# Optimization experiments

Measured on AMD Instinct MI355X. Metric: run time of the kernel, lower is better.

## Reference

```python
import jax, jax.numpy as jnp
import numpy as np

EPS = 1e-6

def setup_inputs() -> dict:
    key = jax.random.key(0)
    ks = jax.random.split(key, 12)
    B, C, H, W = 2, 192, 192, 192
    f = lambda k, s, sc=1.0: jax.random.normal(k, s, dtype=jnp.float32) * sc
    d = {}
    d["x_l"] = f(ks[0], (B, C, H, W))
    d["x_r"] = f(ks[1], (B, C, H, W))
    d["ln_l_w"] = jnp.ones((C,), jnp.float32)
    d["ln_l_b"] = jnp.zeros((C,), jnp.float32)
    d["ln_r_w"] = jnp.ones((C,), jnp.float32)
    d["ln_r_b"] = jnp.zeros((C,), jnp.float32)
    s = C ** -0.5
    d["wq_l"] = f(ks[2], (C, C), s)   # 1x1 conv weights as [out,in]
    d["wq_r"] = f(ks[3], (C, C), s)
    d["wv_l"] = f(ks[4], (C, C), s)
    d["wv_r"] = f(ks[5], (C, C), s)
    d["mlp_w1"] = f(ks[6], (C // 24, C // 3), (C // 3) ** -0.5)
    d["mlp_w2"] = f(ks[7], (C * 2 // 3, C // 24), (C // 24) ** -0.5)
    d["scale_h"] = jnp.ones((1,), jnp.float32)
    d["scale_w"] = jnp.ones((1,), jnp.float32)
    # layer scales are zero-init in the module; use small random so output is nontrivial
    d["ls1"] = f(ks[8], (1, C, 1, 1), 0.1)
    d["ls2"] = f(ks[9], (1, C, 1, 1), 0.1)
    return d

def _ln2d(x, w, b):
    # LayerNorm over channel dim of NCHW
    mu = x.mean(1, keepdims=True)
    var = ((x - mu) ** 2).mean(1, keepdims=True)
    return (x - mu) * jax.lax.rsqrt(var + EPS) * w[None, :, None, None] + b[None, :, None, None]

def _pw(x, w):
    # 1x1 conv, no bias
    return jnp.einsum('bchw,oc->bohw', x, w)

def reference(x_l, x_r, ln_l_w, ln_l_b, ln_r_w, ln_r_b, wq_l, wq_r, wv_l, wv_r,
              mlp_w1, mlp_w2, scale_h, scale_w, ls1, ls2):
    q_l_h, q_l_w, q_l_c = jnp.split(_pw(_ln2d(x_l, ln_l_w, ln_l_b), wq_l), 3, axis=1)
    q_r_h, q_r_w, q_r_c = jnp.split(_pw(_ln2d(x_r, ln_r_w, ln_r_b), wq_r), 3, axis=1)
    v_l_h, v_l_w, v_l_c = jnp.split(_pw(x_l, wv_l), 3, axis=1)
    v_r_h, v_r_w, v_r_c = jnp.split(_pw(x_r, wv_r), 3, axis=1)

    # height axial attention: scores [b, w, h, h']
    attn_h = jnp.einsum('bchw,bcgw->bwhg', q_l_h, q_r_h) * scale_h[0]
    attn_h = jax.nn.softmax(attn_h, axis=-1)
    x_r2l_h = jnp.einsum('bwhg,bcgw->bchw', attn_h, v_r_h)           # [b,c,h,w]
    x_l2r_h = jnp.einsum('bwhg,bchw->bcgw', attn_h, v_l_h)           # attn^T @ v_l

    # width axial attention: scores [b, h, w, w'] (softmax applied separately per direction)
    attn_w = jnp.einsum('bchw,bchv->bhwv', q_l_w, q_r_w) * scale_w[0]
    a1 = jax.nn.softmax(attn_w, axis=-1)
    x_r2l_w = jnp.einsum('bhwv,bchv->bchw', a1, v_r_w)
    a2 = jax.nn.softmax(jnp.swapaxes(attn_w, -1, -2), axis=-1)       # [b,h,v,w]
    x_l2r_w = jnp.einsum('bhvw,bchw->bchv', a2, v_l_w)

    # channel SE branch: sum of the two channel queries, GAP, bottleneck MLP
    p = (q_l_c + q_r_c).mean(axis=(2, 3))                            # [b, c]
    h1 = jax.nn.relu(p @ mlp_w1.T)                                   # [b, c//8]
    a = jax.nn.softmax(h1 @ mlp_w2.T, axis=1)                        # softmax over 2c channels jointly
    attn_l_c, attn_r_c = jnp.split(a, 2, axis=1)
    x_r2l_c = attn_l_c[:, :, None, None] * v_l_c
    x_l2r_c = attn_r_c[:, :, None, None] * v_r_c

    x_r2l = jnp.concatenate([x_r2l_h, x_r2l_w, x_r2l_c], axis=1)
    x_l2r = jnp.concatenate([x_l2r_h, x_l2r_w, x_l2r_c], axis=1)
    out_l = x_r2l * ls1 + x_l
    out_r = x_l2r * ls2 + x_r
    return (out_l, out_r)
```

## Files before the change

### kernel.cpp

```cpp
#include <hip/hip_runtime.h>
#include <stdint.h>

#define NN 36864
#define PL 7077888
#define PL64 2359296
#define TOT 14155776

typedef unsigned short ushort_t;
typedef __attribute__((ext_vector_type(8))) __bf16 bf16x8;
typedef __attribute__((ext_vector_type(4))) float f32x4;
typedef __attribute__((ext_vector_type(4))) unsigned int u32x4;

__device__ __forceinline__ ushort_t f2bf(float f) {
  unsigned int u = __builtin_bit_cast(unsigned int, f);
  u = (u + 0x7FFFu + ((u >> 16) & 1u)) >> 16;
  return (ushort_t)u;
}
__device__ __forceinline__ float bf2f(ushort_t h) {
  unsigned int u = ((unsigned int)h) << 16;
  return __builtin_bit_cast(float, u);
}
__device__ __forceinline__ bf16x8 lds8(const ushort_t* p) {
  return __builtin_bit_cast(bf16x8, *(const u32x4*)p);
}
__device__ __forceinline__ f32x4 mfma16(bf16x8 a, bf16x8 b, f32x4 c) {
  return __builtin_amdgcn_mfma_f32_16x16x32_bf16(a, b, c, 0, 0, 0);
}
__device__ __forceinline__ unsigned cvtpk(float lo, float hi) {
  unsigned r;
  asm("v_cvt_pk_bf16_f32 %0, %1, %2" : "=v"(r) : "v"(lo), "v"(hi));
  return r;
}

__global__ void k_prep(const float* __restrict__ wq, const float* __restrict__ wv,
                       const float* __restrict__ lnw, const float* __restrict__ lnb,
                       ushort_t* __restrict__ W, float* __restrict__ ab) {
  __shared__ float sa[3], sb[3];
  int r = blockIdx.x, t = threadIdx.x;
  if (r < 192) {
    float w  = wq[r*192 + t];
    float lw = lnw[t], lb = lnb[t];
    W[r*192 + t] = f2bf(w * lw);
    float av = w * lb, bv = -w * lw;
    #pragma unroll
    for (int off = 1; off < 64; off <<= 1) {
      av += __shfl_xor(av, off);
      bv += __shfl_xor(bv, off);
    }
    if ((t & 63) == 0) { sa[t >> 6] = av; sb[t >> 6] = bv; }
    __syncthreads();
    if (t == 0) { ab[r] = sa[0]+sa[1]+sa[2]; ab[192 + r] = sb[0]+sb[1]+sb[2]; }
  } else {
    W[r*192 + t] = f2bf(wv[(r-192)*192 + t]);
  }
}

__global__ void k_stats(const float* __restrict__ xl, const float* __restrict__ xr,
                        float* __restrict__ stl, float* __restrict__ str) {
  int bid = blockIdx.x;
  int side = bid / 288, rem = bid % 288;
  int b = rem / 144, nb = rem % 144;
  const float* x = side ? xr : xl;
  float* st = side ? str : stl;
  int n = nb*256 + threadIdx.x;
  const float* p = x + (size_t)b*PL + n;
  float s = 0.f, s2 = 0.f;
  #pragma unroll 4
  for (int c = 0; c < 192; ++c) { float v = p[(size_t)c*NN]; s += v; s2 += v*v; }
  float mu = s * (1.f/192.f);
  float var = s2 * (1.f/192.f) - mu*mu;
  st[(b*2+0)*NN + n] = mu;
  st[(b*2+1)*NN + n] = rsqrtf(var + 1e-6f);
}

__global__ __launch_bounds__(512, 4) void k_proj(
    const float* __restrict__ xl, const float* __restrict__ xr,
    const ushort_t* __restrict__ Wl, const ushort_t* __restrict__ Wr,
    const float* __restrict__ abl, const float* __restrict__ abr,
    const float* __restrict__ stl, const float* __restrict__ str,
    ushort_t* __restrict__ qhTl, ushort_t* __restrict__ qhTr,
    ushort_t* __restrict__ qwTl, ushort_t* __restrict__ qwTr,
    ushort_t* __restrict__ Vl, ushort_t* __restrict__ Vr,
    float* __restrict__ gpart) {
  __shared__ union {
    struct { ushort_t A[2][4096]; ushort_t B[2][6144]; } kl;
    struct { ushort_t T[192*72]; float gsum[64]; } ep;
  } sm;

  const int side = blockIdx.y;
  const float*    x  = side ? xr  : xl;
  const ushort_t* W  = side ? Wr  : Wl;
  const float*    ab = side ? abr : abl;
  const float*    st = side ? str : stl;
  ushort_t* qhT = side ? qhTr : qhTl;
  ushort_t* qwT = side ? qwTr : qwTl;
  ushort_t* V   = side ? Vr   : Vl;

  const int bx = blockIdx.x;
  const int mb = bx % 3;
  const int bh = bx / 3;
  const int b  = bh / 192, h = bh % 192;
  const int m0 = mb * 128;
  const int tid = threadIdx.x;
  const int wave = tid >> 6, lane = tid & 63, lr = lane & 15, lg = lane >> 4;
  const int wm = wave >> 2, wn = wave & 3;

  const int kg0 = tid / 192, n_0 = tid - kg0 * 192;
  const int id1 = 512 + (tid & 255);
  const int kg1 = id1 / 192, n_1 = id1 - kg1 * 192;
  const float* xb0 = x + (size_t)b*PL + (size_t)(kg0*8)*NN + h*192 + n_0;
  const float* xb1 = x + (size_t)b*PL + (size_t)(kg1*8)*NN + h*192 + n_1;
  const int bw0 = n_0*32 + 8*(kg0 ^ ((n_0 >> 1) & 3));
  const int bw1 = n_1*32 + 8*(kg1 ^ ((n_1 >> 1) & 3));
  const int am = tid >> 2, akb = tid & 3;
  const ushort_t* wsrc = W + (m0 + am)*192 + akb*8;
  const int aw = am*32 + 8*(akb ^ ((am >> 1) & 3));
  const int slotR = 8 * (lg ^ ((lr >> 1) & 3));

  const f32x4 fz = {0.f, 0.f, 0.f, 0.f};
  f32x4 acc[4][3];
  #pragma unroll
  for (int mf = 0; mf < 4; ++mf)
    #pragma unroll
    for (int nf = 0; nf < 3; ++nf) acc[mf][nf] = fz;

  {
    u32x4 aV = *(const u32x4*)wsrc;
    float g0[8], g1[8];
    #pragma unroll
    for (int j = 0; j < 8; ++j) g0[j] = xb0[(size_t)j*NN];
    if (tid < 256) {
      #pragma unroll
      for (int j = 0; j < 8; ++j) g1[j] = xb1[(size_t)j*NN];
    }
    *(u32x4*)&sm.kl.A[0][aw] = aV;
    union { ushort_t us[8]; u32x4 v; } t0;
    #pragma unroll
    for (int j = 0; j < 8; ++j) t0.us[j] = f2bf(g0[j]);
    *(u32x4*)&sm.kl.B[0][bw0] = t0.v;
    if (tid < 256) {
      union { ushort_t us[8]; u32x4 v; } t1;
      #pragma unroll
      for (int j = 0; j < 8; ++j) t1.us[j] = f2bf(g1[j]);
      *(u32x4*)&sm.kl.B[0][bw1] = t1.v;
    }
  }
  __syncthreads();

  for (int ks = 0; ks < 6; ++ks) {
    const int cur = ks & 1, nxt = cur ^ 1;
    u32x4 aN;
    float g0[8], g1[8];
    if (ks < 5) {
      const int k0n = (ks + 1) * 32;
      aN = *(const u32x4*)(wsrc + k0n);
      #pragma unroll
      for (int j = 0; j < 8; ++j) g0[j] = xb0[(size_t)(k0n + j)*NN];
      if (tid < 256) {
        #pragma unroll
        for (int j = 0; j < 8; ++j) g1[j] = xb1[(size_t)(k0n + j)*NN];
      }
    }
    bf16x8 bfr[3];
    #pragma unroll
    for (int nf = 0; nf < 3; ++nf)
      bfr[nf] = lds8(&sm.kl.B[cur][(wn*48 + nf*16 + lr)*32 + slotR]);
    #pragma unroll
    for (int mf = 0; mf < 4; ++mf) {
      bf16x8 af = lds8(&sm.kl.A[cur][(wm*64 + mf*16 + lr)*32 + slotR]);
      #pragma unroll
      for (int nf = 0; nf < 3; ++nf) acc[mf][nf] = mfma16(af, bfr[nf], acc[mf][nf]);
    }
    if (ks < 5) {
      *(u32x4*)&sm.kl.A[nxt][aw] = aN;
      union { ushort_t us[8]; u32x4 v; } t0;
      #pragma unroll
      for (int j = 0; j < 8; ++j) t0.us[j] = f2bf(g0[j]);
      *(u32x4*)&sm.kl.B[nxt][bw0] = t0.v;
      if (tid < 256) {
        union { ushort_t us[8]; u32x4 v; } t1;
        #pragma unroll
        for (int j = 0; j < 8; ++j) t1.us[j] = f2bf(g1[j]);
        *(u32x4*)&sm.kl.B[nxt][bw1] = t1.v;
      }
    }
    __syncthreads();
  }

  if (mb == 0) {
    float rst[3], mrs[3];
    #pragma unroll
    for (int nf = 0; nf < 3; ++nf) {
      int n_ = h*192 + wn*48 + nf*16 + lr;
      float rs = st[(b*2+1)*NN + n_];
      rst[nf] = rs;
      mrs[nf] = st[(b*2+0)*NN + n_] * rs;
    }
    #pragma unroll
    for (int mf = 0; mf < 4; ++mf) {
      #pragma unroll
      for (int i = 0; i < 4; ++i) {
        int m = wm*64 + mf*16 + lg*4 + i;
        float a_ = ab[m], bb = ab[192 + m];
        #pragma unroll
        for (int nf = 0; nf < 3; ++nf)
          acc[mf][nf][i] = acc[mf][nf][i]*rst[nf] + bb*mrs[nf] + a_;
      }
    }
    if (wm == 0) {
      #pragma unroll
      for (int mf = 0; mf < 4; ++mf)
        #pragma unroll
        for (int nf = 0; nf < 3; ++nf)
          #pragma unroll
          for (int i = 0; i < 4; ++i)
            sm.ep.T[(wn*48 + nf*16 + lr)*72 + mf*16 + lg*4 + i] = f2bf(acc[mf][nf][i]);
    }
    __syncthreads();
    #pragma unroll
    for (int p = 0; p < 3; ++p) {
      int id = p*512 + tid, n = id >> 3, c8 = id & 7;
      u32x4 v = *(const u32x4*)&sm.ep.T[n*72 + c8*8];
      *(u32x4*)&qhT[(((size_t)b*192 + n)*192 + h)*64 + c8*8] = v;
    }
    __syncthreads();
    if (wm == 1) {
      #pragma unroll
      for (int mf = 0; mf < 4; ++mf)
        #pragma unroll
        for (int nf = 0; nf < 3; ++nf)
          #pragma unroll
          for (int i = 0; i < 4; ++i)
            sm.ep.T[(wn*48 + nf*16 + lr)*72 + mf*16 + lg*4 + i] = f2bf(acc[mf][nf][i]);
    }
    __syncthreads();
    #pragma unroll
    for (int p = 0; p < 3; ++p) {
      int id = p*512 + tid, n = id >> 3, c8 = id & 7;
      u32x4 v = *(const u32x4*)&sm.ep.T[n*72 + c8*8];
      *(u32x4*)&qwT[(((size_t)b*192 + h)*192 + n)*64 + c8*8] = v;
    }
  } else {
    if (mb == 1 && tid < 64) sm.ep.gsum[tid] = 0.f;
    __syncthreads();
    if (mb == 1) {
      if (wm == 0) {
        float rst[3], mrs[3];
        #pragma unroll
        for (int nf = 0; nf < 3; ++nf) {
          int n_ = h*192 + wn*48 + nf*16 + lr;
          float rs = st[(b*2+1)*NN + n_];
          rst[nf] = rs;
          mrs[nf] = st[(b*2+0)*NN + n_] * rs;
        }
        #pragma unroll
        for (int mf = 0; mf < 4; ++mf) {
          #pragma unroll
          for (int i = 0; i < 4; ++i) {
            int m = 128 + mf*16 + lg*4 + i;
            float a_ = ab[m], bb = ab[192 + m];
            float part = 0.f;
            #pragma unroll
            for (int nf = 0; nf < 3; ++nf)
              part += acc[mf][nf][i]*rst[nf] + bb*mrs[nf] + a_;
            #pragma unroll
            for (int off = 1; off < 16; off <<= 1) part += __shfl_xor(part, off);
            if (lr == 0) atomicAdd(&sm.ep.gsum[mf*16 + lg*4 + i], part);
          }
        }
      } else {
        #pragma unroll
        for (int mf = 0; mf < 4; ++mf)
          #pragma unroll
          for (int i = 0; i < 4; ++i) {
            int c = mf*16 + lg*4 + i;
            #pragma unroll
            for (int nf = 0; nf < 3; ++nf)
              V[((size_t)b*192 + c)*NN + h*192 + wn*48 + nf*16 + lr] = f2bf(acc[mf][nf][i]);
          }
      }
      __syncthreads();
      if (tid < 64) gpart[(((size_t)side*2 + b)*192 + h)*64 + tid] = sm.ep.gsum[tid];
    } else {
      #pragma unroll
      for (int mf = 0; mf < 4; ++mf)
        #pragma unroll
        for (int i = 0; i < 4; ++i) {
          int c = 64 + wm*64 + mf*16 + lg*4 + i;
          #pragma unroll
          for (int nf = 0; nf < 3; ++nf)
            V[((size_t)b*192 + c)*NN + h*192 + wn*48 + nf*16 + lr] = f2bf(acc[mf][nf][i]);
        }
    }
  }
}

__global__ void k_repack_v(const ushort_t* __restrict__ Vl, const ushort_t* __restrict__ Vr,
                           ushort_t* __restrict__ vhTl, ushort_t* __restrict__ vhTr) {
  __shared__ ushort_t Ls[64*72];
  const ushort_t* V = blockIdx.y ? Vr : Vl;
  ushort_t* out = blockIdx.y ? vhTr : vhTl;
  int bx = blockIdx.x;
  int b = bx / 576, rem = bx % 576;
  int c = rem / 9, tt = rem % 9;
  int h0 = (tt/3)*64, w0 = (tt%3)*64;
  int tid = threadIdx.x;
  #pragma unroll
  for (int i = 0; i < 2; ++i) {
    int idx = tid + 256*i;
    int hh = idx >> 3, wb = idx & 7;
    *(u32x4*)&Ls[hh*72 + wb*8] =
      *(const u32x4*)&V[(size_t)(b*192 + c)*NN + (h0+hh)*192 + w0 + wb*8];
  }
  __syncthreads();
  #pragma unroll
  for (int i = 0; i < 2; ++i) {
    int idx = tid + 256*i;
    int ww = idx >> 3, hb = idx & 7;
    union { ushort_t us[8]; u32x4 v; } tu;
    #pragma unroll
    for (int j = 0; j < 8; ++j) tu.us[j] = Ls[(hb*8+j)*72 + ww];
    *(u32x4*)&out[(size_t)(b*64 + c)*NN + (w0+ww)*192 + h0 + hb*8] = tu.v;
  }
}

__global__ __launch_bounds__(256, 2) void k_attn(
    const ushort_t* __restrict__ qhTl, const ushort_t* __restrict__ qhTr,
    const ushort_t* __restrict__ qwTl, const ushort_t* __restrict__ qwTr,
    const ushort_t* __restrict__ Vl,  const ushort_t* __restrict__ Vr,
    const ushort_t* __restrict__ vhTl, const ushort_t* __restrict__ vhTr,
    const float* __restrict__ sch, const float* __restrict__ scw,
    ushort_t* __restrict__ Oh1, ushort_t* __restrict__ Oh2,
    ushort_t* __restrict__ Ow1, ushort_t* __restrict__ Ow2) {
  __shared__ ushort_t Qsl[192*64];
  __shared__ ushort_t Qsr[192*64];
  __shared__ ushort_t Vs[64*192];
  __shared__ float md[192*2];

  const int tid = threadIdx.x;
  const int wave = tid >> 6, lane = tid & 63, lr = lane & 15, lg = lane >> 4;
  const int bx = blockIdx.x;
  const int mode = bx / 384;
  const int b = (bx % 384) / 192, s0 = bx % 192;
  const float scl = (mode ? scw : sch)[0];

  const ushort_t* ql = (mode ? qwTl : qhTl) + (size_t)(b*192 + s0)*12288;
  const ushort_t* qr = (mode ? qwTr : qhTr) + (size_t)(b*192 + s0)*12288;
  const ushort_t* vr = mode ? Vr + (size_t)(b*192 + 64)*NN + s0*192
                            : vhTr + (size_t)b*PL64 + s0*192;
  const ushort_t* vl = mode ? Vl + (size_t)(b*192 + 64)*NN + s0*192
                            : vhTl + (size_t)b*PL64 + s0*192;
  ushort_t* o1 = (mode ? Ow1 : Oh1) + (size_t)b*PL64 + s0*192;
  ushort_t* o2 = (mode ? Ow2 : Oh2) + (size_t)b*PL64 + s0*192;

  #pragma unroll
  for (int i = 0; i < 6; ++i) {
    int idx = tid + 256*i;
    int r = idx >> 3, sl = idx & 7;
    int dq = r*64 + ((sl ^ (r & 7)) << 3);
    *(u32x4*)&Qsl[dq] = *(const u32x4*)&ql[idx*8];
    *(u32x4*)&Qsr[dq] = *(const u32x4*)&qr[idx*8];
    int c = idx / 24, gs = idx % 24;
    *(u32x4*)&Vs[c*192 + ((gs ^ (c & 7)) << 3)] = *(const u32x4*)&vr[(size_t)c*NN + gs*8];
  }
  __syncthreads();

  const f32x4 fz = {0.f, 0.f, 0.f, 0.f};
  f32x4 acc[12][3];
  unsigned pk[3][12][2];

  auto qk = [&](bool swap) {
    const ushort_t* A  = swap ? Qsl : Qsr;
    const ushort_t* Bq = swap ? Qsr : Qsl;
    #pragma unroll
    for (int mf = 0; mf < 12; ++mf)
      #pragma unroll
      for (int nf = 0; nf < 3; ++nf) acc[mf][nf] = fz;
    #pragma unroll
    for (int kh = 0; kh < 2; ++kh) {
      bf16x8 bq[3];
      #pragma unroll
      for (int nf = 0; nf < 3; ++nf) {
        int r = wave*48 + nf*16 + lr;
        bq[nf] = lds8(&Bq[r*64 + (((kh*4 + lg) ^ (r & 7)) << 3)]);
      }
      #pragma unroll
      for (int mf = 0; mf < 12; ++mf) {
        int r = mf*16 + lr;
        bf16x8 aq = lds8(&A[r*64 + (((kh*4 + lg) ^ (r & 7)) << 3)]);
        #pragma unroll
        for (int nf = 0; nf < 3; ++nf) acc[mf][nf] = mfma16(aq, bq[nf], acc[mf][nf]);
      }
    }
  };

  auto smpack = [&](bool store_md) {
    #pragma unroll
    for (int nf = 0; nf < 3; ++nf) {
      float mx = -3.4e38f;
      #pragma unroll
      for (int mf = 0; mf < 12; ++mf)
        #pragma unroll
        for (int i = 0; i < 4; ++i) {
          float v = acc[mf][nf][i] * scl;
          acc[mf][nf][i] = v;
          mx = fmaxf(mx, v);
        }
      mx = fmaxf(mx, __shfl_xor(mx, 16));
      mx = fmaxf(mx, __shfl_xor(mx, 32));
      float den = 0.f;
      #pragma unroll
      for (int mf = 0; mf < 12; ++mf)
        #pragma unroll
        for (int i = 0; i < 4; ++i) {
          float e = __expf(acc[mf][nf][i] - mx);
          acc[mf][nf][i] = e;
          den += e;
        }
      den += __shfl_xor(den, 16);
      den += __shfl_xor(den, 32);
      float rd = 1.f / den;
      if (store_md && lg == 0) {
        int col = wave*48 + nf*16 + lr;
        md[col*2] = mx; md[col*2+1] = rd;
      }
      #pragma unroll
      for (int mf = 0; mf < 12; ++mf) {
        pk[nf][mf][0] = cvtpk(acc[mf][nf][0]*rd, acc[mf][nf][1]*rd);
        pk[nf][mf][1] = cvtpk(acc[mf][nf][2]*rd, acc[mf][nf][3]*rd);
      }
    }
  };

  auto pv = [&](ushort_t* op) {
    f32x4 o[4][3];
    #pragma unroll
    for (int mf = 0; mf < 4; ++mf)
      #pragma unroll
      for (int nf = 0; nf < 3; ++nf) o[mf][nf] = fz;
    const int sA = lr + 32*(lg & 1), sB = sA + 16;
    const bool hi = (lg >> 1) != 0;
    #pragma unroll
    for (int ks = 0; ks < 6; ++ks) {
      bf16x8 av[4];
      #pragma unroll
      for (int mf = 0; mf < 4; ++mf) {
        int c = mf*16 + lr;
        av[mf] = lds8(&Vs[c*192 + (((4*ks + lg) ^ (c & 7)) << 3)]);
      }
      #pragma unroll
      for (int nf = 0; nf < 3; ++nf) {
        unsigned w0a = (unsigned)__shfl((int)pk[nf][2*ks  ][0], sA);
        unsigned w0b = (unsigned)__shfl((int)pk[nf][2*ks+1][0], sA);
        unsigned w1a = (unsigned)__shfl((int)pk[nf][2*ks  ][1], sA);
        unsigned w1b = (unsigned)__shfl((int)pk[nf][2*ks+1][1], sA);
        unsigned w2a = (unsigned)__shfl((int)pk[nf][2*ks  ][0], sB);
        unsigned w2b = (unsigned)__shfl((int)pk[nf][2*ks+1][0], sB);
        unsigned w3a = (unsigned)__shfl((int)pk[nf][2*ks  ][1], sB);
        unsigned w3b = (unsigned)__shfl((int)pk[nf][2*ks+1][1], sB);
        u32x4 wv = { hi ? w0b : w0a, hi ? w1b : w1a, hi ? w2b : w2a, hi ? w3b : w3a };
        bf16x8 bp = __builtin_bit_cast(bf16x8, wv);
        #pragma unroll
        for (int mf = 0; mf < 4; ++mf) o[mf][nf] = mfma16(av[mf], bp, o[mf][nf]);
      }
    }
    #pragma unroll
    for (int mf = 0; mf < 4; ++mf)
      #pragma unroll
      for (int i = 0; i < 4; ++i)
        #pragma unroll
        for (int nf = 0; nf < 3; ++nf)
          op[(size_t)(mf*16 + lg*4 + i)*NN + wave*48 + nf*16 + lr] = f2bf(o[mf][nf][i]);
  };

  qk(false);
  smpack(true);
  pv(o1);

  u32x4 vlr[6];
  #pragma unroll
  for (int i = 0; i < 6; ++i) {
    int idx = tid + 256*i;
    int c = idx / 24, gs = idx % 24;
    vlr[i] = *(const u32x4*)&vl[(size_t)c*NN + gs*8];
  }
  __syncthreads();

  qk(true);
  #pragma unroll
  for (int i = 0; i < 6; ++i) {
    int idx = tid + 256*i;
    int c = idx / 24, gs = idx % 24;
    *(u32x4*)&Vs[c*192 + ((gs ^ (c & 7)) << 3)] = vlr[i];
  }
  if (mode == 0) {
    #pragma unroll
    for (int mf = 0; mf < 12; ++mf)
      #pragma unroll
      for (int i = 0; i < 4; ++i) {
        int row = mf*16 + lg*4 + i;
        float m_ = md[row*2], rd_ = md[row*2+1];
        #pragma unroll
        for (int nf = 0; nf < 3; ++nf)
          acc[mf][nf][i] = __expf(acc[mf][nf][i]*scl - m_) * rd_;
      }
    #pragma unroll
    for (int nf = 0; nf < 3; ++nf)
      #pragma unroll
      for (int mf = 0; mf < 12; ++mf) {
        pk[nf][mf][0] = cvtpk(acc[mf][nf][0], acc[mf][nf][1]);
        pk[nf][mf][1] = cvtpk(acc[mf][nf][2], acc[mf][nf][3]);
      }
  } else {
    smpack(false);
  }
  __syncthreads();
  pv(o2);
}

__global__ void k_se(const float* __restrict__ gpart, const float* __restrict__ w1,
                     const float* __restrict__ w2, float* __restrict__ sea) {
  __shared__ float p[2][64];
  __shared__ float h1[2][8];
  __shared__ float lgt[2][128];
  __shared__ float mred[2], dred[2];
  int t = threadIdx.x;
  if (t < 128) {
    int b = t >> 6, c = t & 63;
    float s = 0.f;
    for (int side = 0; side < 2; ++side)
      for (int h = 0; h < 192; ++h)
        s += gpart[(((size_t)side*2 + b)*192 + h)*64 + c];
    p[b][c] = s * (1.f/36864.f);
  }
  __syncthreads();
  if (t < 16) {
    int bb = t >> 3, j = t & 7;
    float s = 0.f;
    for (int k = 0; k < 64; ++k) s += p[bb][k] * w1[j*64 + k];
    h1[bb][j] = fmaxf(s, 0.f);
  }
  __syncthreads();
  {
    int bb = t >> 7, o = t & 127;
    float s = 0.f;
    #pragma unroll
    for (int j = 0; j < 8; ++j) s += h1[bb][j] * w2[o*8 + j];
    lgt[bb][o] = s;
  }
  __syncthreads();
  if (t < 2) {
    float mx = -3.4e38f;
    for (int o = 0; o < 128; ++o) mx = fmaxf(mx, lgt[t][o]);
    float d = 0.f;
    for (int o = 0; o < 128; ++o) d += __expf(lgt[t][o] - mx);
    mred[t] = mx; dred[t] = d;
  }
  __syncthreads();
  {
    int bb = t >> 7, o = t & 127;
    sea[bb*128 + o] = __expf(lgt[bb][o] - mred[bb]) / dred[bb];
  }
}

__global__ void k_ep_h(const ushort_t* __restrict__ Oh1, const ushort_t* __restrict__ Oh2,
                       const float* __restrict__ xl, const float* __restrict__ xr,
                       const float* __restrict__ ls1, const float* __restrict__ ls2,
                       float* __restrict__ out) {
  __shared__ ushort_t Ls[64*72];
  int dir = blockIdx.y;
  const ushort_t* O = dir ? Oh2 : Oh1;
  const float* xin = dir ? xr : xl;
  float lsv = (dir ? ls2 : ls1)[blockIdx.x % 576 / 9];
  int bx = blockIdx.x;
  int b = bx / 576, rem = bx % 576;
  int c = rem / 9, tt = rem % 9;
  int h0 = (tt/3)*64, w0 = (tt%3)*64;
  int tid = threadIdx.x;
  const ushort_t* Ob = O + (size_t)(b*64 + c)*NN;
  const float* xb = xin + (size_t)(b*192 + c)*NN;
  float* ob = out + (size_t)dir*TOT + (size_t)(b*192 + c)*NN;
  #pragma unroll
  for (int i = 0; i < 2; ++i) {
    int idx = tid + 256*i;
    int ww = idx >> 3, hb = idx & 7;
    *(u32x4*)&Ls[ww*72 + hb*8] = *(const u32x4*)&Ob[(w0+ww)*192 + h0 + hb*8];
  }
  __syncthreads();
  #pragma unroll
  for (int i = 0; i < 2; ++i) {
    int idx = tid + 256*i;
    int hh = idx >> 3, wb = idx & 7;
    int base = (h0+hh)*192 + w0 + wb*8;
    f32x4 xa = *(const f32x4*)&xb[base];
    f32x4 xc = *(const f32x4*)&xb[base + 4];
    f32x4 r0, r1;
    #pragma unroll
    for (int j = 0; j < 4; ++j) r0[j] = bf2f(Ls[(wb*8+j)*72 + hh])*lsv + xa[j];
    #pragma unroll
    for (int j = 0; j < 4; ++j) r1[j] = bf2f(Ls[(wb*8+4+j)*72 + hh])*lsv + xc[j];
    *(f32x4*)&ob[base] = r0;
    *(f32x4*)&ob[base + 4] = r1;
  }
}

__global__ void k_ep_wc(const ushort_t* __restrict__ Ow1, const ushort_t* __restrict__ Ow2,
                        const ushort_t* __restrict__ Vl, const ushort_t* __restrict__ Vr,
                        const float* __restrict__ sea,
                        const float* __restrict__ xl, const float* __restrict__ xr,
                        const float* __restrict__ ls1, const float* __restrict__ ls2,
                        float* __restrict__ out) {
  int gid = blockIdx.x;
  int tile = gid % 18;
  int c128 = (gid / 18) % 128;
  int b = (gid / (18*128)) % 2;
  int dir = gid / (18*128*2);
  int cg = 64 + c128;
  const float* xin = dir ? xr : xl;
  float lsv = (dir ? ls2 : ls1)[cg];
  int n0 = tile*2048 + threadIdx.x*8;
  size_t xo = (size_t)(b*192 + cg)*NN + n0;
  const ushort_t* src;
  float mult;
  if (c128 < 64) {
    src = (dir ? Ow2 : Ow1) + (size_t)(b*64 + c128)*NN + n0;
    mult = lsv;
  } else {
    int cc = c128 - 64;
    src = (dir ? Vr : Vl) + (size_t)(b*192 + 128 + cc)*NN + n0;
    mult = lsv * sea[b*128 + dir*64 + cc];
  }
  u32x4 sv = *(const u32x4*)src;
  const ushort_t* sp = (const ushort_t*)&sv;
  f32x4 xa = *(const f32x4*)&xin[xo];
  f32x4 xb = *(const f32x4*)&xin[xo + 4];
  f32x4 r0, r1;
  #pragma unroll
  for (int j = 0; j < 4; ++j) r0[j] = bf2f(sp[j])*mult + xa[j];
  #pragma unroll
  for (int j = 0; j < 4; ++j) r1[j] = bf2f(sp[4+j])*mult + xb[j];
  float* ob = out + (size_t)dir*TOT;
  *(f32x4*)&ob[xo] = r0;
  *(f32x4*)&ob[xo + 4] = r1;
}

extern "C" void kernel_launch(void* const* d_in, const int* in_sizes, int n_in,
                              void* d_out, int out_size, void* d_ws, size_t ws_size,
                              hipStream_t stream) {
  const float* x_l  = (const float*)d_in[0];
  const float* x_r  = (const float*)d_in[1];
  const float* lnlw = (const float*)d_in[2];
  const float* lnlb = (const float*)d_in[3];
  const float* lnrw = (const float*)d_in[4];
  const float* lnrb = (const float*)d_in[5];
  const float* wq_l = (const float*)d_in[6];
  const float* wq_r = (const float*)d_in[7];
  const float* wv_l = (const float*)d_in[8];
  const float* wv_r = (const float*)d_in[9];
  const float* w1   = (const float*)d_in[10];
  const float* w2   = (const float*)d_in[11];
  const float* sch  = (const float*)d_in[12];
  const float* scw  = (const float*)d_in[13];
  const float* ls1  = (const float*)d_in[14];
  const float* ls2  = (const float*)d_in[15];
  float* out = (float*)d_out;

  char* ws = (char*)d_ws;
  size_t off = 0;
  auto alloc = [&](size_t bytes) {
    char* p = ws + off;
    off += (bytes + 255) & ~(size_t)255;
    return p;
  };
  ushort_t* Vl   = (ushort_t*)alloc((size_t)2*192*NN*2);
  ushort_t* Vr   = (ushort_t*)alloc((size_t)2*192*NN*2);
  ushort_t* qhTl = (ushort_t*)alloc((size_t)2*64*NN*2);
  ushort_t* qhTr = (ushort_t*)alloc((size_t)2*64*NN*2);
  ushort_t* qwTl = (ushort_t*)alloc((size_t)2*64*NN*2);
  ushort_t* qwTr = (ushort_t*)alloc((size_t)2*64*NN*2);
  ushort_t* vhTl = (ushort_t*)alloc((size_t)2*64*NN*2);
  ushort_t* vhTr = (ushort_t*)alloc((size_t)2*64*NN*2);
  ushort_t* Oh1  = (ushort_t*)alloc((size_t)2*64*NN*2);
  ushort_t* Oh2  = (ushort_t*)alloc((size_t)2*64*NN*2);
  ushort_t* Ow1  = (ushort_t*)alloc((size_t)2*64*NN*2);
  ushort_t* Ow2  = (ushort_t*)alloc((size_t)2*64*NN*2);
  ushort_t* Wl   = (ushort_t*)alloc((size_t)384*192*2);
  ushort_t* Wr   = (ushort_t*)alloc((size_t)384*192*2);
  float* abl = (float*)alloc(384*4);
  float* abr = (float*)alloc(384*4);
  float* stl = (float*)alloc((size_t)4*NN*4);
  float* str = (float*)alloc((size_t)4*NN*4);
  float* gpart = (float*)alloc((size_t)2*2*192*64*4);
  float* sea = (float*)alloc(2*128*4);
  (void)in_sizes; (void)n_in; (void)out_size; (void)ws_size;

  k_prep<<<384, 192, 0, stream>>>(wq_l, wv_l, lnlw, lnlb, Wl, abl);
  k_prep<<<384, 192, 0, stream>>>(wq_r, wv_r, lnrw, lnrb, Wr, abr);
  k_stats<<<576, 256, 0, stream>>>(x_l, x_r, stl, str);
  k_proj<<<dim3(1152, 2), 512, 0, stream>>>(x_l, x_r, Wl, Wr, abl, abr, stl, str,
                                            qhTl, qhTr, qwTl, qwTr, Vl, Vr, gpart);
  k_repack_v<<<dim3(1152, 2), 256, 0, stream>>>(Vl, Vr, vhTl, vhTr);
  k_attn<<<768, 256, 0, stream>>>(qhTl, qhTr, qwTl, qwTr, Vl, Vr, vhTl, vhTr,
                                  sch, scw, Oh1, Oh2, Ow1, Ow2);
  k_se<<<1, 256, 0, stream>>>(gpart, w1, w2, sea);
  k_ep_h<<<dim3(1152, 2), 256, 0, stream>>>(Oh1, Oh2, x_l, x_r, ls1, ls2, out);
  k_ep_wc<<<9216, 256, 0, stream>>>(Ow1, Ow2, Vl, Vr, sea, x_l, x_r, ls1, ls2, out);
}
```

Before: 231.4 us.

## Fuse LN stats into projection, restage attention outputs, merge epilogues

Removes the separate layer-norm statistics kernel by accumulating per-pixel sum and sum-of-squares inside the projection's K loop and reducing them in shared memory. The attention kernel now stages its outputs through swizzled LDS and writes them in a new channel-last layout with 16-byte stores, and it raises wave priority around the MFMA blocks. The two epilogue kernels are merged into one per-row kernel that reads this layout. Launch bounds on the projection kernel drop to 2 blocks per SM, which may lower occupancy but saves a full read pass over both inputs and one launch.

```diff
diff --git a/kernel.cpp b/kernel.cpp
--- a/kernel.cpp
+++ b/kernel.cpp
@@ -10,6 +10,7 @@
 typedef __attribute__((ext_vector_type(8))) __bf16 bf16x8;
 typedef __attribute__((ext_vector_type(4))) float f32x4;
 typedef __attribute__((ext_vector_type(4))) unsigned int u32x4;
+typedef __attribute__((ext_vector_type(2))) unsigned int u32x2;
 
 __device__ __forceinline__ ushort_t f2bf(float f) {
   unsigned int u = __builtin_bit_cast(unsigned int, f);
@@ -55,29 +56,10 @@
   }
 }
 
-__global__ void k_stats(const float* __restrict__ xl, const float* __restrict__ xr,
-                        float* __restrict__ stl, float* __restrict__ str) {
-  int bid = blockIdx.x;
-  int side = bid / 288, rem = bid % 288;
-  int b = rem / 144, nb = rem % 144;
-  const float* x = side ? xr : xl;
-  float* st = side ? str : stl;
-  int n = nb*256 + threadIdx.x;
-  const float* p = x + (size_t)b*PL + n;
-  float s = 0.f, s2 = 0.f;
-  #pragma unroll 4
-  for (int c = 0; c < 192; ++c) { float v = p[(size_t)c*NN]; s += v; s2 += v*v; }
-  float mu = s * (1.f/192.f);
-  float var = s2 * (1.f/192.f) - mu*mu;
-  st[(b*2+0)*NN + n] = mu;
-  st[(b*2+1)*NN + n] = rsqrtf(var + 1e-6f);
-}
-
-__global__ __launch_bounds__(512, 4) void k_proj(
+__global__ __launch_bounds__(512, 2) void k_proj(
     const float* __restrict__ xl, const float* __restrict__ xr,
     const ushort_t* __restrict__ Wl, const ushort_t* __restrict__ Wr,
     const float* __restrict__ abl, const float* __restrict__ abr,
-    const float* __restrict__ stl, const float* __restrict__ str,
     ushort_t* __restrict__ qhTl, ushort_t* __restrict__ qhTr,
     ushort_t* __restrict__ qwTl, ushort_t* __restrict__ qwTr,
     ushort_t* __restrict__ Vl, ushort_t* __restrict__ Vr,
@@ -86,12 +68,13 @@
     struct { ushort_t A[2][4096]; ushort_t B[2][6144]; } kl;
     struct { ushort_t T[192*72]; float gsum[64]; } ep;
   } sm;
+  __shared__ float spart[4][192], spart2[4][192];
+  __shared__ float smu[192], srs[192];
 
   const int side = blockIdx.y;
   const float*    x  = side ? xr  : xl;
   const ushort_t* W  = side ? Wr  : Wl;
   const float*    ab = side ? abr : abl;
-  const float*    st = side ? str : stl;
   ushort_t* qhT = side ? qhTr : qhTl;
   ushort_t* qwT = side ? qwTr : qwTl;
   ushort_t* V   = side ? Vr   : Vl;
@@ -124,6 +107,8 @@
     #pragma unroll
     for (int nf = 0; nf < 3; ++nf) acc[mf][nf] = fz;
 
+  float sA0 = 0.f, sB0 = 0.f, sA1 = 0.f, sB1 = 0.f;
+
   {
     u32x4 aV = *(const u32x4*)wsrc;
     float g0[8], g1[8];
@@ -136,12 +121,12 @@
     *(u32x4*)&sm.kl.A[0][aw] = aV;
     union { ushort_t us[8]; u32x4 v; } t0;
     #pragma unroll
-    for (int j = 0; j < 8; ++j) t0.us[j] = f2bf(g0[j]);
+    for (int j = 0; j < 8; ++j) { t0.us[j] = f2bf(g0[j]); sA0 += g0[j]; sB0 += g0[j]*g0[j]; }
     *(u32x4*)&sm.kl.B[0][bw0] = t0.v;
     if (tid < 256) {
       union { ushort_t us[8]; u32x4 v; } t1;
       #pragma unroll
-      for (int j = 0; j < 8; ++j) t1.us[j] = f2bf(g1[j]);
+      for (int j = 0; j < 8; ++j) { t1.us[j] = f2bf(g1[j]); sA1 += g1[j]; sB1 += g1[j]*g1[j]; }
       *(u32x4*)&sm.kl.B[0][bw1] = t1.v;
     }
   }
@@ -175,26 +160,40 @@
       *(u32x4*)&sm.kl.A[nxt][aw] = aN;
       union { ushort_t us[8]; u32x4 v; } t0;
       #pragma unroll
-      for (int j = 0; j < 8; ++j) t0.us[j] = f2bf(g0[j]);
+      for (int j = 0; j < 8; ++j) { t0.us[j] = f2bf(g0[j]); sA0 += g0[j]; sB0 += g0[j]*g0[j]; }
       *(u32x4*)&sm.kl.B[nxt][bw0] = t0.v;
       if (tid < 256) {
         union { ushort_t us[8]; u32x4 v; } t1;
         #pragma unroll
-        for (int j = 0; j < 8; ++j) t1.us[j] = f2bf(g1[j]);
+        for (int j = 0; j < 8; ++j) { t1.us[j] = f2bf(g1[j]); sA1 += g1[j]; sB1 += g1[j]*g1[j]; }
         *(u32x4*)&sm.kl.B[nxt][bw1] = t1.v;
       }
     }
     __syncthreads();
   }
+
+  spart[kg0][n_0] = sA0; spart2[kg0][n_0] = sB0;
+  if (tid < 256) { spart[kg1][n_1] = sA1; spart2[kg1][n_1] = sB1; }
+  if (mb == 1 && tid >= 448) sm.ep.gsum[tid - 448] = 0.f;
+  __syncthreads();
+  if (tid < 192) {
+    float s  = spart[0][tid] + spart[1][tid] + spart[2][tid] + spart[3][tid];
+    float s2 = spart2[0][tid] + spart2[1][tid] + spart2[2][tid] + spart2[3][tid];
+    float mu = s * (1.f/192.f);
+    float var = s2 * (1.f/192.f) - mu*mu;
+    smu[tid] = mu;
+    srs[tid] = rsqrtf(var + 1e-6f);
+  }
+  __syncthreads();
 
   if (mb == 0) {
     float rst[3], mrs[3];
     #pragma unroll
     for (int nf = 0; nf < 3; ++nf) {
-      int n_ = h*192 + wn*48 + nf*16 + lr;
-      float rs = st[(b*2+1)*NN + n_];
+      int n_ = wn*48 + nf*16 + lr;
+      float rs = srs[n_];
       rst[nf] = rs;
-      mrs[nf] = st[(b*2+0)*NN + n_] * rs;
+      mrs[nf] = smu[n_] * rs;
     }
     #pragma unroll
     for (int mf = 0; mf < 4; ++mf) {
@@ -241,17 +240,15 @@
       *(u32x4*)&qwT[(((size_t)b*192 + h)*192 + n)*64 + c8*8] = v;
     }
   } else {
-    if (mb == 1 && tid < 64) sm.ep.gsum[tid] = 0.f;
-    __syncthreads();
     if (mb == 1) {
       if (wm == 0) {
         float rst[3], mrs[3];
         #pragma unroll
         for (int nf = 0; nf < 3; ++nf) {
-          int n_ = h*192 + wn*48 + nf*16 + lr;
-          float rs = st[(b*2+1)*NN + n_];
+          int n_ = wn*48 + nf*16 + lr;
+          float rs = srs[n_];
           rst[nf] = rs;
-          mrs[nf] = st[(b*2+0)*NN + n_] * rs;
+          mrs[nf] = smu[n_] * rs;
         }
         #pragma unroll
         for (int mf = 0; mf < 4; ++mf) {
@@ -350,8 +347,8 @@
                             : vhTr + (size_t)b*PL64 + s0*192;
   const ushort_t* vl = mode ? Vl + (size_t)(b*192 + 64)*NN + s0*192
                             : vhTl + (size_t)b*PL64 + s0*192;
-  ushort_t* o1 = (mode ? Ow1 : Oh1) + (size_t)b*PL64 + s0*192;
-  ushort_t* o2 = (mode ? Ow2 : Oh2) + (size_t)b*PL64 + s0*192;
+  ushort_t* og1 = (mode ? Ow1 : Oh1) + (size_t)(b*192 + s0)*12288;
+  ushort_t* og2 = (mode ? Ow2 : Oh2) + (size_t)(b*192 + s0)*12288;
 
   #pragma unroll
   for (int i = 0; i < 6; ++i) {
@@ -376,6 +373,7 @@
     for (int mf = 0; mf < 12; ++mf)
       #pragma unroll
       for (int nf = 0; nf < 3; ++nf) acc[mf][nf] = fz;
+    __builtin_amdgcn_s_setprio(1);
     #pragma unroll
     for (int kh = 0; kh < 2; ++kh) {
       bf16x8 bq[3];
@@ -392,6 +390,7 @@
         for (int nf = 0; nf < 3; ++nf) acc[mf][nf] = mfma16(aq, bq[nf], acc[mf][nf]);
       }
     }
+    __builtin_amdgcn_s_setprio(0);
   };
 
   auto smpack = [&](bool store_md) {
@@ -432,7 +431,7 @@
     }
   };
 
-  auto pv = [&](ushort_t* op) {
+  auto pv = [&](unsigned obf[4][3][2]) {
     f32x4 o[4][3];
     #pragma unroll
     for (int mf = 0; mf < 4; ++mf)
@@ -440,6 +439,7 @@
       for (int nf = 0; nf < 3; ++nf) o[mf][nf] = fz;
     const int sA = lr + 32*(lg & 1), sB = sA + 16;
     const bool hi = (lg >> 1) != 0;
+    __builtin_amdgcn_s_setprio(1);
     #pragma unroll
     for (int ks = 0; ks < 6; ++ks) {
       bf16x8 av[4];
@@ -464,18 +464,45 @@
         for (int mf = 0; mf < 4; ++mf) o[mf][nf] = mfma16(av[mf], bp, o[mf][nf]);
       }
     }
+    __builtin_amdgcn_s_setprio(0);
     #pragma unroll
     for (int mf = 0; mf < 4; ++mf)
       #pragma unroll
-      for (int i = 0; i < 4; ++i)
-        #pragma unroll
-        for (int nf = 0; nf < 3; ++nf)
-          op[(size_t)(mf*16 + lg*4 + i)*NN + wave*48 + nf*16 + lr] = f2bf(o[mf][nf][i]);
+      for (int nf = 0; nf < 3; ++nf) {
+        obf[mf][nf][0] = cvtpk(o[mf][nf][0], o[mf][nf][1]);
+        obf[mf][nf][1] = cvtpk(o[mf][nf][2], o[mf][nf][3]);
+      }
+  };
+
+  auto owrite = [&](unsigned obf[4][3][2]) {
+    char* Ot = (char*)Qsl;
+    #pragma unroll
+    for (int mf = 0; mf < 4; ++mf)
+      #pragma unroll
+      for (int nf = 0; nf < 3; ++nf) {
+        int col = wave*48 + nf*16 + lr;
+        int byte = col*128 + ((mf*32 + lg*8) ^ ((col & 7) << 4));
+        u32x2 v = { obf[mf][nf][0], obf[mf][nf][1] };
+        *(u32x2*)(Ot + byte) = v;
+      }
+  };
+
+  auto ostore = [&](ushort_t* og) {
+    const char* Ot = (const char*)Qsl;
+    #pragma unroll
+    for (int it = 0; it < 6; ++it) {
+      int id = tid + 256*it;
+      int col = id >> 3, s = id & 7;
+      int byte = col*128 + ((s*16) ^ ((col & 7) << 4));
+      u32x4 v = *(const u32x4*)(Ot + byte);
+      *(u32x4*)&og[(size_t)col*64 + s*8] = v;
+    }
   };
 
   qk(false);
   smpack(true);
-  pv(o1);
+  unsigned o1bf[4][3][2];
+  pv(o1bf);
 
   u32x4 vlr[6];
   #pragma unroll
@@ -484,15 +511,18 @@
     int c = idx / 24, gs = idx % 24;
     vlr[i] = *(const u32x4*)&vl[(size_t)c*NN + gs*8];
   }
-  __syncthreads();
 
   qk(true);
+  __syncthreads();
+
+  owrite(o1bf);
   #pragma unroll
   for (int i = 0; i < 6; ++i) {
     int idx = tid + 256*i;
     int c = idx / 24, gs = idx % 24;
     *(u32x4*)&Vs[c*192 + ((gs ^ (c & 7)) << 3)] = vlr[i];
   }
+
   if (mode == 0) {
     #pragma unroll
     for (int mf = 0; mf < 12; ++mf)
@@ -515,7 +545,14 @@
     smpack(false);
   }
   __syncthreads();
-  pv(o2);
+
+  ostore(og1);
+  unsigned o2bf[4][3][2];
+  pv(o2bf);
+  __syncthreads();
+  owrite(o2bf);
+  __syncthreads();
+  ostore(og2);
 }
 
 __global__ void k_se(const float* __restrict__ gpart, const float* __restrict__ w1,
@@ -563,85 +600,99 @@
   }
 }
 
-__global__ void k_ep_h(const ushort_t* __restrict__ Oh1, const ushort_t* __restrict__ Oh2,
-                       const float* __restrict__ xl, const float* __restrict__ xr,
-                       const float* __restrict__ ls1, const float* __restrict__ ls2,
-                       float* __restrict__ out) {
-  __shared__ ushort_t Ls[64*72];
-  int dir = blockIdx.y;
-  const ushort_t* O = dir ? Oh2 : Oh1;
+__global__ __launch_bounds__(256, 4) void k_ep(
+    const ushort_t* __restrict__ Oh1, const ushort_t* __restrict__ Oh2,
+    const ushort_t* __restrict__ Ow1, const ushort_t* __restrict__ Ow2,
+    const ushort_t* __restrict__ Vl, const ushort_t* __restrict__ Vr,
+    const float* __restrict__ sea,
+    const float* __restrict__ xl, const float* __restrict__ xr,
+    const float* __restrict__ ls1, const float* __restrict__ ls2,
+    float* __restrict__ out) {
+  __shared__ ushort_t T[192*64];
+  const int gid = blockIdx.x;
+  const int h = gid % 192;
+  const int b = (gid / 192) % 2;
+  const int dir = gid / 384;
+  const int tid = threadIdx.x;
   const float* xin = dir ? xr : xl;
-  float lsv = (dir ? ls2 : ls1)[blockIdx.x % 576 / 9];
-  int bx = blockIdx.x;
-  int b = bx / 576, rem = bx % 576;
-  int c = rem / 9, tt = rem % 9;
-  int h0 = (tt/3)*64, w0 = (tt%3)*64;
-  int tid = threadIdx.x;
-  const ushort_t* Ob = O + (size_t)(b*64 + c)*NN;
-  const float* xb = xin + (size_t)(b*192 + c)*NN;
-  float* ob = out + (size_t)dir*TOT + (size_t)(b*192 + c)*NN;
+  const float* ls  = dir ? ls2 : ls1;
+  const ushort_t* Oh = dir ? Oh2 : Oh1;
+  const ushort_t* Ow = dir ? Ow2 : Ow1;
+  const ushort_t* Vv = dir ? Vr  : Vl;
+  float* outp = out + (size_t)dir*TOT;
+
+  const int c0 = (tid / 24) * 8, wseg = tid % 24, w0 = wseg * 8;
+  const int Srd = (wseg & 7) << 4;
+
+  auto flush = [&](int cbase) {
+    if (tid < 192) {
+      u32x4 r[8];
+      #pragma unroll
+      for (int j = 0; j < 8; ++j)
+        r[j] = *(const u32x4*)((const char*)T + (w0 + j)*128 + ((c0*2) ^ Srd));
+      #pragma unroll
+      for (int k = 0; k < 8; ++k) {
+        int c = cbase + c0 + k;
+        float lsv = ls[c];
+        size_t oo = (size_t)(b*192 + c)*NN + h*192 + w0;
+        f32x4 xa = *(const f32x4*)&xin[oo];
+        f32x4 xb2 = *(const f32x4*)&xin[oo + 4];
+        f32x4 r0, r1;
+        #pragma unroll
+        for (int j = 0; j < 4; ++j) r0[j] = bf2f(((const ushort_t*)&r[j])[k])*lsv + xa[j];
+        #pragma unroll
+        for (int j = 0; j < 4; ++j) r1[j] = bf2f(((const ushort_t*)&r[4+j])[k])*lsv + xb2[j];
+        *(f32x4*)&outp[oo] = r0;
+        *(f32x4*)&outp[oo + 4] = r1;
+      }
+    }
+  };
+
+  {
+    const ushort_t* ohb = Oh + ((size_t)b*192*192 + h)*64;
+    #pragma unroll
+    for (int it = 0; it < 6; ++it) {
+      int id = tid + 256*it;
+      int w = id >> 3, s = id & 7;
+      u32x4 v = *(const u32x4*)&ohb[(size_t)w*12288 + s*8];
+      *(u32x4*)((char*)T + w*128 + ((s*16) ^ (((w >> 3) & 7) << 4))) = v;
+    }
+  }
+  __syncthreads();
+  flush(0);
+  __syncthreads();
+
+  {
+    const ushort_t* owb = Ow + ((size_t)b*192 + h)*12288;
+    #pragma unroll
+    for (int it = 0; it < 6; ++it) {
+      int id = tid + 256*it;
+      int w = id >> 3, s = id & 7;
+      u32x4 v = *(const u32x4*)&owb[id*8];
+      *(u32x4*)((char*)T + w*128 + ((s*16) ^ (((w >> 3) & 7) << 4))) = v;
+    }
+  }
+  __syncthreads();
+  flush(64);
+
   #pragma unroll
-  for (int i = 0; i < 2; ++i) {
-    int idx = tid + 256*i;
-    int ww = idx >> 3, hb = idx & 7;
-    *(u32x4*)&Ls[ww*72 + hb*8] = *(const u32x4*)&Ob[(w0+ww)*192 + h0 + hb*8];
-  }
-  __syncthreads();
-  #pragma unroll
-  for (int i = 0; i < 2; ++i) {
-    int idx = tid + 256*i;
-    int hh = idx >> 3, wb = idx & 7;
-    int base = (h0+hh)*192 + w0 + wb*8;
-    f32x4 xa = *(const f32x4*)&xb[base];
-    f32x4 xc = *(const f32x4*)&xb[base + 4];
+  for (int it = 0; it < 6; ++it) {
+    int id = tid + 256*it;
+    int cc = id / 24, ws = (id % 24) * 8;
+    float lsv = ls[128 + cc] * sea[b*128 + dir*64 + cc];
+    size_t oo = (size_t)(b*192 + 128 + cc)*NN + h*192 + ws;
+    u32x4 sv = *(const u32x4*)&Vv[(size_t)(b*192 + 128 + cc)*NN + h*192 + ws];
+    const ushort_t* sp = (const ushort_t*)&sv;
+    f32x4 xa = *(const f32x4*)&xin[oo];
+    f32x4 xb2 = *(const f32x4*)&xin[oo + 4];
     f32x4 r0, r1;
     #pragma unroll
-    for (int j = 0; j < 4; ++j) r0[j] = bf2f(Ls[(wb*8+j)*72 + hh])*lsv + xa[j];
-    #pragma unroll
-    for (int j = 0; j < 4; ++j) r1[j] = bf2f(Ls[(wb*8+4+j)*72 + hh])*lsv + xc[j];
-    *(f32x4*)&ob[base] = r0;
-    *(f32x4*)&ob[base + 4] = r1;
-  }
-}
-
-__global__ void k_ep_wc(const ushort_t* __restrict__ Ow1, const ushort_t* __restrict__ Ow2,
-                        const ushort_t* __restrict__ Vl, const ushort_t* __restrict__ Vr,
-                        const float* __restrict__ sea,
-                        const float* __restrict__ xl, const float* __restrict__ xr,
-                        const float* __restrict__ ls1, const float* __restrict__ ls2,
-                        float* __restrict__ out) {
-  int gid = blockIdx.x;
-  int tile = gid % 18;
-  int c128 = (gid / 18) % 128;
-  int b = (gid / (18*128)) % 2;
-  int dir = gid / (18*128*2);
-  int cg = 64 + c128;
-  const float* xin = dir ? xr : xl;
-  float lsv = (dir ? ls2 : ls1)[cg];
-  int n0 = tile*2048 + threadIdx.x*8;
-  size_t xo = (size_t)(b*192 + cg)*NN + n0;
-  const ushort_t* src;
-  float mult;
-  if (c128 < 64) {
-    src = (dir ? Ow2 : Ow1) + (size_t)(b*64 + c128)*NN + n0;
-    mult = lsv;
-  } else {
-    int cc = c128 - 64;
-    src = (dir ? Vr : Vl) + (size_t)(b*192 + 128 + cc)*NN + n0;
-    mult = lsv * sea[b*128 + dir*64 + cc];
-  }
-  u32x4 sv = *(const u32x4*)src;
-  const ushort_t* sp = (const ushort_t*)&sv;
-  f32x4 xa = *(const f32x4*)&xin[xo];
-  f32x4 xb = *(const f32x4*)&xin[xo + 4];
-  f32x4 r0, r1;
-  #pragma unroll
-  for (int j = 0; j < 4; ++j) r0[j] = bf2f(sp[j])*mult + xa[j];
-  #pragma unroll
-  for (int j = 0; j < 4; ++j) r1[j] = bf2f(sp[4+j])*mult + xb[j];
-  float* ob = out + (size_t)dir*TOT;
-  *(f32x4*)&ob[xo] = r0;
-  *(f32x4*)&ob[xo + 4] = r1;
+    for (int j = 0; j < 4; ++j) r0[j] = bf2f(sp[j])*lsv + xa[j];
+    #pragma unroll
+    for (int j = 0; j < 4; ++j) r1[j] = bf2f(sp[4+j])*lsv + xb2[j];
+    *(f32x4*)&outp[oo] = r0;
+    *(f32x4*)&outp[oo + 4] = r1;
+  }
 }
 
 extern "C" void kernel_launch(void* const* d_in, const int* in_sizes, int n_in,
@@ -688,21 +739,18 @@
   ushort_t* Wr   = (ushort_t*)alloc((size_t)384*192*2);
   float* abl = (float*)alloc(384*4);
   float* abr = (float*)alloc(384*4);
-  float* stl = (float*)alloc((size_t)4*NN*4);
-  float* str = (float*)alloc((size_t)4*NN*4);
   float* gpart = (float*)alloc((size_t)2*2*192*64*4);
   float* sea = (float*)alloc(2*128*4);
   (void)in_sizes; (void)n_in; (void)out_size; (void)ws_size;
 
   k_prep<<<384, 192, 0, stream>>>(wq_l, wv_l, lnlw, lnlb, Wl, abl);
   k_prep<<<384, 192, 0, stream>>>(wq_r, wv_r, lnrw, lnrb, Wr, abr);
-  k_stats<<<576, 256, 0, stream>>>(x_l, x_r, stl, str);
-  k_proj<<<dim3(1152, 2), 512, 0, stream>>>(x_l, x_r, Wl, Wr, abl, abr, stl, str,
+  k_proj<<<dim3(1152, 2), 512, 0, stream>>>(x_l, x_r, Wl, Wr, abl, abr,
                                             qhTl, qhTr, qwTl, qwTr, Vl, Vr, gpart);
   k_repack_v<<<dim3(1152, 2), 256, 0, stream>>>(Vl, Vr, vhTl, vhTr);
   k_attn<<<768, 256, 0, stream>>>(qhTl, qhTr, qwTl, qwTr, Vl, Vr, vhTl, vhTr,
                                   sch, scw, Oh1, Oh2, Ow1, Ow2);
   k_se<<<1, 256, 0, stream>>>(gpart, w1, w2, sea);
-  k_ep_h<<<dim3(1152, 2), 256, 0, stream>>>(Oh1, Oh2, x_l, x_r, ls1, ls2, out);
-  k_ep_wc<<<9216, 256, 0, stream>>>(Ow1, Ow2, Vl, Vr, sea, x_l, x_r, ls1, ls2, out);
-}
+  k_ep<<<768, 256, 0, stream>>>(Oh1, Oh2, Ow1, Ow2, Vl, Vr, sea,
+                                x_l, x_r, ls1, ls2, out);
+}
```

After: 246.0 us. 1.06x slower.
